# Performance work log

Hardware: AMD Instinct MI355X
Metric: run time of the kernel (lower is better)

The kernel has to match this reference:

```python
import jax, jax.numpy as jnp
import numpy as np

T, B, IN, OUT = 32, 16, 64, 64
L, W, S = 4096, 64, 3          # mem_length, mem_width, shifting_size
READ_SIZE = W + 3 + S           # k, beta, g, gamma, s
WRITE_SIZE = W + 3 + S + 2 * W  # addressing params + erase + add


def setup_inputs() -> dict:
    key = jax.random.key(0)
    k1, k2 = jax.random.split(key)
    inputs = jax.random.normal(k1, (T, B, IN), dtype=jnp.float32)
    Wc = jax.random.normal(k2, (IN + OUT + W, OUT + READ_SIZE + WRITE_SIZE), dtype=jnp.float32) * 0.05
    bc = jnp.zeros((OUT + READ_SIZE + WRITE_SIZE,), dtype=jnp.float32)
    return {"inputs": inputs, "Wc": Wc, "bc": bc}


def _get_w(params, w_prev, memory):
    # params: [B, W+3+S]; w_prev: [B, L]; memory: [B, L, W]
    k = params[:, :W]
    beta = jax.nn.softplus(params[:, W])[:, None]
    g = jax.nn.sigmoid(params[:, W + 1])[:, None]
    gamma = jax.nn.softplus(params[:, W + 2])[:, None] + 1.0
    s = jax.nn.softmax(params[:, -S:], axis=-1)
    eps = 1e-14
    norm_k = jnp.sqrt(jnp.sum(k * k, axis=-1, keepdims=True) + eps)    # [B,1]
    norm_mem = jnp.sqrt(jnp.sum(memory * memory, axis=-1) + eps)       # [B,L]
    K = jnp.einsum('blw,bw->bl', memory, k) / (norm_mem * norm_k)      # cosine sim
    w_c = jax.nn.softmax(K * beta, axis=-1)
    w_g = w_c * g + (1.0 - g) * w_prev
    # circular shift: w_tilde[i] = sum_j s[j] * w_g[(i + j - left) mod L]
    left = S // 2
    shifted = jnp.stack([jnp.roll(w_g, left - j, axis=1) for j in range(S)], axis=-1)  # [B,L,S]
    w_tilde = jnp.einsum('bls,bs->bl', shifted, s)
    w = jnp.power(w_tilde, gamma)   # sharpen, gamma >= 1
    return w / jnp.sum(w, axis=1, keepdims=True)


def reference(inputs, Wc, bc):
    Bsz = inputs.shape[1]
    r0 = jnp.zeros((Bsz, W), jnp.float32)
    o0 = jnp.zeros((Bsz, OUT), jnp.float32)
    w0 = jnp.zeros((Bsz, L), jnp.float32).at[:, 0].set(1.0)  # one-hot init weights
    m0 = jnp.zeros((Bsz, L, W), jnp.float32)

    def step(carry, x_t):
        r, out, rw, ww, mem = carry
        co = jnp.concatenate([x_t, out, r], axis=1) @ Wc + bc  # linear controller
        out = co[:, :OUT]
        rp = co[:, OUT:OUT + READ_SIZE]
        wp = co[:, -WRITE_SIZE:]
        # read head (uses pre-write memory)
        rw = _get_w(rp, rw, mem)
        r = jnp.einsum('blw,bl->bw', mem, rw)
        # write head: address with same memory, then erase/add
        ww = _get_w(wp[:, :-2 * W], ww, mem)
        e = jax.nn.sigmoid(wp[:, -2 * W:-W])
        a = wp[:, -W:]
        mem = mem * (1.0 - ww[:, :, None] * e[:, None, :]) + ww[:, :, None] * a[:, None, :]
        return (r, out, rw, ww, mem), out

    _, outs = jax.lax.scan(step, (r0, o0, w0, w0, m0), inputs)
    return outs  # [T, B, OUT]
```

## Files before the change

kernel.cpp:

```cpp
#include <hip/hip_runtime.h>

#define T_STEPS 32
#define BATCH   16
#define NBPB    8
#define NBLK    (BATCH * NBPB)
#define NTHR    1024
#define LSL     512
#define MSTR    65
#define NIN     192
#define CO      332

#define OFF_CTR   0
#define OFF_SSUM  512
#define OFF_RSUM  (OFF_SSUM + BATCH * T_STEPS * 4)
#define OFF_HE    (OFF_RSUM + BATCH * T_STEPS * 64)
#define OFF_HP    (OFF_HE + BATCH * T_STEPS * NBPB * 4)
#define COMM_FLOATS (OFF_HP + BATCH * (T_STEPS + 1) * NBPB * 4)

__device__ __forceinline__ float waveSum(float v) {
#pragma unroll
  for (int off = 32; off > 0; off >>= 1) v += __shfl_xor(v, off, 64);
  return v;
}
__device__ __forceinline__ float sigmoidf(float x) { return 1.f / (1.f + __expf(-x)); }
__device__ __forceinline__ float softplusf(float x) { return x > 15.f ? x : log1pf(__expf(x)); }
__device__ __forceinline__ float aload(const float* p) {
  return __hip_atomic_load(p, __ATOMIC_RELAXED, __HIP_MEMORY_SCOPE_AGENT);
}
__device__ __forceinline__ void astore(float* p, float v) {
  __hip_atomic_store(p, v, __ATOMIC_RELAXED, __HIP_MEMORY_SCOPE_AGENT);
}

__device__ __forceinline__ void gbar(unsigned* c, unsigned expected) {
  __syncthreads();
  if (threadIdx.x == 0) {
    atomicAdd(c, 1u);
    while (__hip_atomic_load(c, __ATOMIC_RELAXED, __HIP_MEMORY_SCOPE_AGENT) < expected)
      __builtin_amdgcn_s_sleep(1);
  }
  __syncthreads();
}

__global__ void __launch_bounds__(NTHR, 1) ntm_kernel(
    const float* __restrict__ inp, const float* __restrict__ Wc,
    const float* __restrict__ bcv, float* __restrict__ dout,
    float* __restrict__ comm)
{
  const int b   = blockIdx.x & 15;
  const int g   = blockIdx.x >> 4;
  const int tid = threadIdx.x;
  const int wv  = tid >> 6;
  const int lane = tid & 63;

  __shared__ float mem[LSL * MSTR];
  __shared__ float wpR[LSL], wpW[LSL];
  __shared__ float wbR[LSL], wbW[LSL];
  __shared__ float erR[LSL], erW[LSL];
  __shared__ float xin[NIN], kr[64], kw[64], psc[12], elds[64], alds[64];
  __shared__ float outb[2][64], scrA[16], scrB[16], red[8], rpart[64];
  __shared__ float edge[8], coef[12];

  unsigned* ctr = (unsigned*)comm + b * 32;

  for (int i = tid; i < LSL * MSTR; i += NTHR) mem[i] = 0.f;
  if (tid < LSL) { wpR[tid] = 0.f; wpW[tid] = 0.f; }
  if (g == 0 && tid == 0) { wpR[0] = 1.f; wpW[0] = 1.f; }
  if (tid < 64) { outb[0][tid] = 0.f; outb[1][tid] = 0.f; }
  {
    float* hp0 = comm + OFF_HP + ((size_t)(b * (T_STEPS + 1) + 0) * NBPB + g) * 4;
    if (tid == 0)       { float v = (g == 0) ? 1.f : 0.f; astore(hp0 + 0, v); astore(hp0 + 2, v); }
    if (tid == LSL - 1) { astore(hp0 + 1, 0.f); astore(hp0 + 3, 0.f); }
  }
  unsigned expct = NBPB;
  gbar(ctr, expct);

  for (int t = 0; t < T_STEPS; ++t) {
    float* sS  = comm + OFF_SSUM + (size_t)(b * T_STEPS + t) * 4;
    float* rS  = comm + OFF_RSUM + (size_t)(b * T_STEPS + t) * 64;
    float* hE  = comm + OFF_HE + ((size_t)(b * T_STEPS + t) * NBPB + g) * 4;
    float* hPn = comm + OFF_HP + ((size_t)(b * (T_STEPS + 1) + t + 1) * NBPB + g) * 4;

    if (tid < 64)       xin[tid] = inp[((size_t)t * BATCH + b) * 64 + tid];
    else if (tid < 128) xin[tid] = outb[(t + 1) & 1][tid - 64];
    else if (tid < 192) {
      if (t == 0) xin[tid] = 0.f;
      else {
        const float* sP = comm + OFF_SSUM + (size_t)(b * T_STEPS + t - 1) * 4;
        const float* rP = comm + OFF_RSUM + (size_t)(b * T_STEPS + t - 1) * 64;
        xin[tid] = aload(rP + (tid - 128)) / aload(sP + 2);
      }
    }
    __syncthreads();

    if (tid < 2 * CO) {
      const int col = tid >> 1, h = tid & 1;
      float acc = h ? 0.f : bcv[col];
      const float* wcp = Wc + col + (size_t)(96 * h) * CO;
#pragma unroll 8
      for (int i = 0; i < 96; ++i) acc = fmaf(xin[96 * h + i], wcp[(size_t)i * CO], acc);
      acc += __shfl_xor(acc, 1, 64);
      if (h == 0) {
        if (col < 64) {
          outb[t & 1][col] = acc;
          if (g == 0) dout[((size_t)t * BATCH + b) * 64 + col] = acc;
        }
        else if (col < 128) kr[col - 64] = acc;
        else if (col < 134) psc[col - 128] = acc;
        else if (col < 198) kw[col - 134] = acc;
        else if (col < 204) psc[6 + (col - 198)] = acc;
        else if (col < 268) elds[col - 204] = sigmoidf(acc);
        else                alds[col - 268] = acc;
      }
    }
    __syncthreads();
    if (wv == 0)      { float v = kr[lane]; float s = waveSum(v * v); if (!lane) red[4] = 1.f / sqrtf(s + 1e-14f); }
    else if (wv == 1) { float v = kw[lane]; float s = waveSum(v * v); if (!lane) red[5] = 1.f / sqrtf(s + 1e-14f); }
    else if (wv == 2 && !lane) { red[6] = softplusf(psc[0]); red[7] = softplusf(psc[6]); }
    __syncthreads();

    {
      const float invnkR = red[4], invnkW = red[5];
      const float betaR = red[6], betaW = red[7];
      const int l = tid >> 1, h = tid & 1;
      const int base = l * MSTR + 32 * h;
      const float* krh = kr + 32 * h;
      const float* kwh = kw + 32 * h;
      float ss = 0.f, dr = 0.f, dw = 0.f;
#pragma unroll 8
      for (int i = 0; i < 32; ++i) {
        float v = mem[base + i];
        ss = fmaf(v, v, ss); dr = fmaf(v, krh[i], dr); dw = fmaf(v, kwh[i], dw);
      }
      ss += __shfl_xor(ss, 1, 64);
      dr += __shfl_xor(dr, 1, 64);
      dw += __shfl_xor(dw, 1, 64);
      float rinv = rsqrtf(ss + 1e-14f);
      float eRv = __expf(betaR * (dr * rinv * invnkR - 1.f));
      float eWv = __expf(betaW * (dw * rinv * invnkW - 1.f));
      if (h == 0) {
        erR[l] = eRv; erW[l] = eWv;
        if (l == 0)       { astore(hE + 0, eRv); astore(hE + 2, eWv); }
        if (l == LSL - 1) { astore(hE + 1, eRv); astore(hE + 3, eWv); }
      }
      float sRl = h ? 0.f : eRv, sWl = h ? 0.f : eWv;
      sRl = waveSum(sRl); sWl = waveSum(sWl);
      if (!lane) { scrA[wv] = sRl; scrB[wv] = sWl; }
      __syncthreads();
      if (tid == 0) {
        float a = 0.f, bb = 0.f;
        for (int j = 0; j < 16; ++j) { a += scrA[j]; bb += scrB[j]; }
        atomicAdd(sS + 0, a); atomicAdd(sS + 1, bb);
      }
    }
    expct += NBPB; gbar(ctr, expct);

    {
      const int gm = (g + NBPB - 1) & 7, gp = (g + 1) & 7;
      if (tid == 0) {
        float invSR = 1.f / aload(sS + 0), invSW = 1.f / aload(sS + 1);
        float gR = sigmoidf(psc[1]); coef[0] = gR * invSR; coef[1] = 1.f - gR;
        coef[2] = softplusf(psc[2]) + 1.f;
        float x0 = psc[3], x1 = psc[4], x2 = psc[5];
        float mx = fmaxf(x0, fmaxf(x1, x2));
        float e0 = __expf(x0 - mx), e1 = __expf(x1 - mx), e2 = __expf(x2 - mx);
        float es = 1.f / (e0 + e1 + e2);
        coef[3] = e0 * es; coef[4] = e1 * es; coef[5] = e2 * es;
        float gW = sigmoidf(psc[7]); coef[6] = gW * invSW; coef[7] = 1.f - gW;
        coef[8] = softplusf(psc[8]) + 1.f;
        float y0 = psc[9], y1 = psc[10], y2 = psc[11];
        float my = fmaxf(y0, fmaxf(y1, y2));
        float f0 = __expf(y0 - my), f1 = __expf(y1 - my), f2 = __expf(y2 - my);
        float fs = 1.f / (f0 + f1 + f2);
        coef[9] = f0 * fs; coef[10] = f1 * fs; coef[11] = f2 * fs;
      }
      if (tid == 1) {
        const float* hEm = comm + OFF_HE + ((size_t)(b * T_STEPS + t) * NBPB + gm) * 4;
        const float* hPm = comm + OFF_HP + ((size_t)(b * (T_STEPS + 1) + t) * NBPB + gm) * 4;
        edge[0] = aload(hEm + 1); edge[1] = aload(hEm + 3);
        edge[2] = aload(hPm + 1); edge[3] = aload(hPm + 3);
      }
      if (tid == 2) {
        const float* hEp = comm + OFF_HE + ((size_t)(b * T_STEPS + t) * NBPB + gp) * 4;
        const float* hPp = comm + OFF_HP + ((size_t)(b * (T_STEPS + 1) + t) * NBPB + gp) * 4;
        edge[4] = aload(hEp + 0); edge[5] = aload(hEp + 2);
        edge[6] = aload(hPp + 0); edge[7] = aload(hPp + 2);
      }
      __syncthreads();

      float pRl = 0.f, pWl = 0.f;
      if (tid < LSL) {
        const float aR = coef[0], bR = coef[1], gaR = coef[2];
        const float sr0 = coef[3], sr1 = coef[4], sr2 = coef[5];
        const float aW = coef[6], bW = coef[7], gaW = coef[8];
        const float sw0 = coef[9], sw1 = coef[10], sw2 = coef[11];

        float erm = tid ? erR[tid - 1] : edge[0];
        float ewm = tid ? erW[tid - 1] : edge[1];
        float prm = tid ? wpR[tid - 1] : edge[2];
        float pwm = tid ? wpW[tid - 1] : edge[3];
        float erp = (tid < LSL - 1) ? erR[tid + 1] : edge[4];
        float ewp = (tid < LSL - 1) ? erW[tid + 1] : edge[5];
        float prp = (tid < LSL - 1) ? wpR[tid + 1] : edge[6];
        float pwp = (tid < LSL - 1) ? wpW[tid + 1] : edge[7];

        float wgm = aR * erm + bR * prm;
        float wg0 = aR * erR[tid] + bR * wpR[tid];
        float wgp = aR * erp + bR * prp;
        float wR = __powf(sr0 * wgm + sr1 * wg0 + sr2 * wgp, gaR);
        float vgm = aW * ewm + bW * pwm;
        float vg0 = aW * erW[tid] + bW * wpW[tid];
        float vgp = aW * ewp + bW * pwp;
        float wW = __powf(sw0 * vgm + sw1 * vg0 + sw2 * vgp, gaW);
        wbR[tid] = wR; wbW[tid] = wW;
        pRl = wR; pWl = wW;
      }
      pRl = waveSum(pRl); pWl = waveSum(pWl);
      if (!lane && wv < 8) { scrA[wv] = pRl; scrB[wv] = pWl; }
      __syncthreads();
      if (tid == 0) {
        float a = 0.f, bb = 0.f;
        for (int j = 0; j < 8; ++j) { a += scrA[j]; bb += scrB[j]; }
        atomicAdd(sS + 2, a); atomicAdd(sS + 3, bb);
      }
      float wbv[8];
#pragma unroll
      for (int k = 0; k < 8; ++k) wbv[k] = wbR[lane + 64 * k];
#pragma unroll
      for (int r2 = 0; r2 < 4; ++r2) {
        const int w = wv * 4 + r2;
        float racc = 0.f;
#pragma unroll
        for (int k = 0; k < 8; ++k)
          racc = fmaf(mem[(lane + 64 * k) * MSTR + w], wbv[k], racc);
        racc = waveSum(racc);
        if (!lane) rpart[w] = racc;
      }
      __syncthreads();
      if (tid < 64) atomicAdd(rS + tid, rpart[tid]);
    }
    expct += NBPB; gbar(ctr, expct);

    {
      if (tid == 0) { red[2] = 1.f / aload(sS + 2); red[3] = 1.f / aload(sS + 3); }
      __syncthreads();
      if (tid < LSL) {
        float nR = wbR[tid] * red[2];
        float nW = wbW[tid] * red[3];
        wpR[tid] = nR; wpW[tid] = nW;
        if (tid == 0)       { astore(hPn + 0, nR); astore(hPn + 2, nW); }
        if (tid == LSL - 1) { astore(hPn + 1, nR); astore(hPn + 3, nW); }
      }
      __syncthreads();
      float wwv[8];
#pragma unroll
      for (int k = 0; k < 8; ++k) wwv[k] = wpW[lane + 64 * k];
#pragma unroll
      for (int r2 = 0; r2 < 4; ++r2) {
        const int w = wv * 4 + r2;
        const float e_w = elds[w], a_w = alds[w];
#pragma unroll
        for (int k = 0; k < 8; ++k) {
          const int idx = (lane + 64 * k) * MSTR + w;
          float v = mem[idx];
          float nv = fmaf(v, -(wwv[k] * e_w), v);
          mem[idx] = fmaf(wwv[k], a_w, nv);
        }
      }
    }
  }
}

extern "C" void kernel_launch(void* const* d_in, const int* in_sizes, int n_in,
                              void* d_out, int out_size, void* d_ws, size_t ws_size,
                              hipStream_t stream) {
  const float* inp = (const float*)d_in[0];
  const float* Wc  = (const float*)d_in[1];
  const float* bcv = (const float*)d_in[2];
  float* dout = (float*)d_out;
  float* comm = (float*)d_ws;

  hipMemsetAsync(comm, 0, (size_t)COMM_FLOATS * sizeof(float), stream);

  void* args[] = { (void*)&inp, (void*)&Wc, (void*)&bcv, (void*)&dout, (void*)&comm };
  hipLaunchCooperativeKernel((void*)ntm_kernel, dim3(NBLK), dim3(NTHR),
                             args, 0, stream);
}
```

Baseline: 712.4 us.

## Restructure NTM step loop with overlapped controller, swizzled float4 memory, split barriers

Rewrites the per-step loop in several ways. Barrier arrival and waiting are split so the next step's controller matmul over input and output runs while waiting for peer blocks. The read-vector part of the Wc weights is cached in registers. Memory rows are padded to 68 floats with an XOR swizzle so float4 LDS accesses avoid bank conflicts. Coefficient computation is spread across threads instead of serialized on single threads, and the read reduction now goes straight to global atomics. Register pressure increases and atomic traffic per block goes up, and the swizzle and reorder add correctness risk.

```diff
diff --git a/kernel.cpp b/kernel.cpp
--- a/kernel.cpp
+++ b/kernel.cpp
@@ -6,7 +6,7 @@
 #define NBLK    (BATCH * NBPB)
 #define NTHR    1024
 #define LSL     512
-#define MSTR    65
+#define MSTR    68
 #define NIN     192
 #define CO      332
 
@@ -30,15 +30,9 @@
 __device__ __forceinline__ void astore(float* p, float v) {
   __hip_atomic_store(p, v, __ATOMIC_RELAXED, __HIP_MEMORY_SCOPE_AGENT);
 }
-
-__device__ __forceinline__ void gbar(unsigned* c, unsigned expected) {
-  __syncthreads();
-  if (threadIdx.x == 0) {
-    atomicAdd(c, 1u);
-    while (__hip_atomic_load(c, __ATOMIC_RELAXED, __HIP_MEMORY_SCOPE_AGENT) < expected)
-      __builtin_amdgcn_s_sleep(1);
-  }
-  __syncthreads();
+__device__ __forceinline__ void spin_until(const unsigned* c, unsigned expected) {
+  while (__hip_atomic_load(c, __ATOMIC_RELAXED, __HIP_MEMORY_SCOPE_AGENT) < expected)
+    __builtin_amdgcn_s_sleep(1);
 }
 
 __global__ void __launch_bounds__(NTHR, 1) ntm_kernel(
@@ -46,90 +40,127 @@
     const float* __restrict__ bcv, float* __restrict__ dout,
     float* __restrict__ comm)
 {
-  const int b   = blockIdx.x & 15;
-  const int g   = blockIdx.x >> 4;
-  const int tid = threadIdx.x;
-  const int wv  = tid >> 6;
+  const int b    = blockIdx.x & 15;
+  const int g    = blockIdx.x >> 4;
+  const int tid  = threadIdx.x;
+  const int wv   = tid >> 6;
   const int lane = tid & 63;
 
-  __shared__ float mem[LSL * MSTR];
+  __shared__ __align__(16) float mem[LSL * MSTR];
   __shared__ float wpR[LSL], wpW[LSL];
   __shared__ float wbR[LSL], wbW[LSL];
   __shared__ float erR[LSL], erW[LSL];
-  __shared__ float xin[NIN], kr[64], kw[64], psc[12], elds[64], alds[64];
-  __shared__ float outb[2][64], scrA[16], scrB[16], red[8], rpart[64];
-  __shared__ float edge[8], coef[12];
+  __shared__ __align__(16) float xin[NIN];
+  __shared__ __align__(16) float kr[64], kw[64], elds[64], alds[64];
+  __shared__ float psc[12], outb[64], scrA[16], scrB[16];
 
   unsigned* ctr = (unsigned*)comm + b * 32;
 
-  for (int i = tid; i < LSL * MSTR; i += NTHR) mem[i] = 0.f;
+  const int col  = tid >> 1;
+  const int hh   = tid & 1;
+  const bool gthr = (col < CO);
+
+  float wreg[32];
+  if (gthr) {
+#pragma unroll
+    for (int i = 0; i < 32; ++i)
+      wreg[i] = Wc[(size_t)(128 + 32 * hh + i) * CO + col];
+  }
+
+  {
+    float4 z4; z4.x = z4.y = z4.z = z4.w = 0.f;
+    float4* m4 = (float4*)mem;
+    for (int i = tid; i < (LSL * MSTR) / 4; i += NTHR) m4[i] = z4;
+  }
   if (tid < LSL) { wpR[tid] = 0.f; wpW[tid] = 0.f; }
   if (g == 0 && tid == 0) { wpR[0] = 1.f; wpW[0] = 1.f; }
-  if (tid < 64) { outb[0][tid] = 0.f; outb[1][tid] = 0.f; }
+  if (tid < 64)            xin[tid] = inp[(size_t)b * 64 + tid];
+  else if (tid < NIN)      xin[tid] = 0.f;
   {
-    float* hp0 = comm + OFF_HP + ((size_t)(b * (T_STEPS + 1) + 0) * NBPB + g) * 4;
-    if (tid == 0)       { float v = (g == 0) ? 1.f : 0.f; astore(hp0 + 0, v); astore(hp0 + 2, v); }
-    if (tid == LSL - 1) { astore(hp0 + 1, 0.f); astore(hp0 + 3, 0.f); }
+    float* hp0 = comm + OFF_HP + ((size_t)(b * (T_STEPS + 1)) * NBPB + g) * 4;
+    if (tid == 0) { float v = (g == 0) ? 1.f : 0.f; astore(hp0 + 0, v); astore(hp0 + 2, v); }
+    if (tid == 1) { astore(hp0 + 1, 0.f); astore(hp0 + 3, 0.f); }
   }
   unsigned expct = NBPB;
-  gbar(ctr, expct);
+  __syncthreads();
+  if (tid == 0)
+    __hip_atomic_fetch_add(ctr, 1u, __ATOMIC_RELEASE, __HIP_MEMORY_SCOPE_AGENT);
+  spin_until(ctr, expct);
+
+  float acc = 0.f;
+  if (gthr) {
+    acc = hh ? 0.f : bcv[col];
+    const float* wcx = Wc + col + (size_t)(64 * hh) * CO;
+#pragma unroll 4
+    for (int q = 0; q < 16; ++q) {
+      const float4 xv = *(const float4*)(xin + 64 * hh + 4 * q);
+      acc = fmaf(xv.x, wcx[(size_t)(4 * q + 0) * CO], acc);
+      acc = fmaf(xv.y, wcx[(size_t)(4 * q + 1) * CO], acc);
+      acc = fmaf(xv.z, wcx[(size_t)(4 * q + 2) * CO], acc);
+      acc = fmaf(xv.w, wcx[(size_t)(4 * q + 3) * CO], acc);
+    }
+#pragma unroll
+    for (int q = 0; q < 8; ++q) {
+      const float4 xv = *(const float4*)(xin + 128 + 32 * hh + 4 * q);
+      acc = fmaf(xv.x, wreg[4 * q + 0], acc);
+      acc = fmaf(xv.y, wreg[4 * q + 1], acc);
+      acc = fmaf(xv.z, wreg[4 * q + 2], acc);
+      acc = fmaf(xv.w, wreg[4 * q + 3], acc);
+    }
+  }
+
+  const int gm = (g + NBPB - 1) & 7, gp = (g + 1) & 7;
 
   for (int t = 0; t < T_STEPS; ++t) {
-    float* sS  = comm + OFF_SSUM + (size_t)(b * T_STEPS + t) * 4;
-    float* rS  = comm + OFF_RSUM + (size_t)(b * T_STEPS + t) * 64;
-    float* hE  = comm + OFF_HE + ((size_t)(b * T_STEPS + t) * NBPB + g) * 4;
-    float* hPn = comm + OFF_HP + ((size_t)(b * (T_STEPS + 1) + t + 1) * NBPB + g) * 4;
-
-    if (tid < 64)       xin[tid] = inp[((size_t)t * BATCH + b) * 64 + tid];
-    else if (tid < 128) xin[tid] = outb[(t + 1) & 1][tid - 64];
-    else if (tid < 192) {
-      if (t == 0) xin[tid] = 0.f;
-      else {
-        const float* sP = comm + OFF_SSUM + (size_t)(b * T_STEPS + t - 1) * 4;
-        const float* rP = comm + OFF_RSUM + (size_t)(b * T_STEPS + t - 1) * 64;
-        xin[tid] = aload(rP + (tid - 128)) / aload(sP + 2);
-      }
-    }
-    __syncthreads();
-
-    if (tid < 2 * CO) {
-      const int col = tid >> 1, h = tid & 1;
-      float acc = h ? 0.f : bcv[col];
-      const float* wcp = Wc + col + (size_t)(96 * h) * CO;
-#pragma unroll 8
-      for (int i = 0; i < 96; ++i) acc = fmaf(xin[96 * h + i], wcp[(size_t)i * CO], acc);
-      acc += __shfl_xor(acc, 1, 64);
-      if (h == 0) {
+    float* sS        = comm + OFF_SSUM + (size_t)(b * T_STEPS + t) * 4;
+    float* rS        = comm + OFF_RSUM + (size_t)(b * T_STEPS + t) * 64;
+    float* hE        = comm + OFF_HE + ((size_t)(b * T_STEPS + t) * NBPB + g) * 4;
+    float* hPn       = comm + OFF_HP + ((size_t)(b * (T_STEPS + 1) + t + 1) * NBPB + g) * 4;
+    const float* hEm = comm + OFF_HE + ((size_t)(b * T_STEPS + t) * NBPB + gm) * 4;
+    const float* hPm = comm + OFF_HP + ((size_t)(b * (T_STEPS + 1) + t) * NBPB + gm) * 4;
+    const float* hEp = comm + OFF_HE + ((size_t)(b * T_STEPS + t) * NBPB + gp) * 4;
+    const float* hPp = comm + OFF_HP + ((size_t)(b * (T_STEPS + 1) + t) * NBPB + gp) * 4;
+
+    if (gthr) {
+      float v = acc + __shfl_xor(acc, 1, 64);
+      if (hh == 0) {
         if (col < 64) {
-          outb[t & 1][col] = acc;
-          if (g == 0) dout[((size_t)t * BATCH + b) * 64 + col] = acc;
+          outb[col] = v;
+          if (g == 0) dout[((size_t)t * BATCH + b) * 64 + col] = v;
         }
-        else if (col < 128) kr[col - 64] = acc;
-        else if (col < 134) psc[col - 128] = acc;
-        else if (col < 198) kw[col - 134] = acc;
-        else if (col < 204) psc[6 + (col - 198)] = acc;
-        else if (col < 268) elds[col - 204] = sigmoidf(acc);
-        else                alds[col - 268] = acc;
-      }
-    }
-    __syncthreads();
-    if (wv == 0)      { float v = kr[lane]; float s = waveSum(v * v); if (!lane) red[4] = 1.f / sqrtf(s + 1e-14f); }
-    else if (wv == 1) { float v = kw[lane]; float s = waveSum(v * v); if (!lane) red[5] = 1.f / sqrtf(s + 1e-14f); }
-    else if (wv == 2 && !lane) { red[6] = softplusf(psc[0]); red[7] = softplusf(psc[6]); }
-    __syncthreads();
-
-    {
-      const float invnkR = red[4], invnkW = red[5];
-      const float betaR = red[6], betaW = red[7];
+        else if (col < 128) kr[col - 64] = v;
+        else if (col < 134) psc[col - 128] = v;
+        else if (col < 198) kw[col - 134] = v;
+        else if (col < 204) psc[6 + (col - 198)] = v;
+        else if (col < 268) elds[col - 204] = sigmoidf(v);
+        else                alds[col - 268] = v;
+      }
+    }
+    __syncthreads();
+
+    {
+      float vr = kr[lane]; float nr = waveSum(vr * vr);
+      float vw = kw[lane]; float nw = waveSum(vw * vw);
+      const float invnkR = rsqrtf(nr + 1e-14f);
+      const float invnkW = rsqrtf(nw + 1e-14f);
+      const float betaR = softplusf(psc[0]), betaW = softplusf(psc[6]);
+
       const int l = tid >> 1, h = tid & 1;
-      const int base = l * MSTR + 32 * h;
-      const float* krh = kr + 32 * h;
-      const float* kwh = kw + 32 * h;
+      const int x4 = ((l >> 3) & 3) << 2;
+      const float* mrow = mem + l * MSTR;
       float ss = 0.f, dr = 0.f, dw = 0.f;
-#pragma unroll 8
-      for (int i = 0; i < 32; ++i) {
-        float v = mem[base + i];
-        ss = fmaf(v, v, ss); dr = fmaf(v, krh[i], dr); dw = fmaf(v, kwh[i], dw);
+#pragma unroll
+      for (int q = 0; q < 8; ++q) {
+        const int gg = 8 * h + q;
+        const float4 v  = *(const float4*)(mrow + ((4 * gg) ^ x4));
+        const float4 ka = *(const float4*)(kr + 4 * gg);
+        const float4 kb = *(const float4*)(kw + 4 * gg);
+        ss = fmaf(v.x, v.x, ss); ss = fmaf(v.y, v.y, ss);
+        ss = fmaf(v.z, v.z, ss); ss = fmaf(v.w, v.w, ss);
+        dr = fmaf(v.x, ka.x, dr); dr = fmaf(v.y, ka.y, dr);
+        dr = fmaf(v.z, ka.z, dr); dr = fmaf(v.w, ka.w, dr);
+        dw = fmaf(v.x, kb.x, dw); dw = fmaf(v.y, kb.y, dw);
+        dw = fmaf(v.z, kb.z, dw); dw = fmaf(v.w, kb.w, dw);
       }
       ss += __shfl_xor(ss, 1, 64);
       dr += __shfl_xor(dr, 1, 64);
@@ -142,131 +173,143 @@
         if (l == 0)       { astore(hE + 0, eRv); astore(hE + 2, eWv); }
         if (l == LSL - 1) { astore(hE + 1, eRv); astore(hE + 3, eWv); }
       }
-      float sRl = h ? 0.f : eRv, sWl = h ? 0.f : eWv;
-      sRl = waveSum(sRl); sWl = waveSum(sWl);
+      float sRl = waveSum(h ? 0.f : eRv);
+      float sWl = waveSum(h ? 0.f : eWv);
       if (!lane) { scrA[wv] = sRl; scrB[wv] = sWl; }
-      __syncthreads();
-      if (tid == 0) {
-        float a = 0.f, bb = 0.f;
-        for (int j = 0; j < 16; ++j) { a += scrA[j]; bb += scrB[j]; }
-        atomicAdd(sS + 0, a); atomicAdd(sS + 1, bb);
-      }
-    }
-    expct += NBPB; gbar(ctr, expct);
-
-    {
-      const int gm = (g + NBPB - 1) & 7, gp = (g + 1) & 7;
-      if (tid == 0) {
-        float invSR = 1.f / aload(sS + 0), invSW = 1.f / aload(sS + 1);
-        float gR = sigmoidf(psc[1]); coef[0] = gR * invSR; coef[1] = 1.f - gR;
-        coef[2] = softplusf(psc[2]) + 1.f;
-        float x0 = psc[3], x1 = psc[4], x2 = psc[5];
-        float mx = fmaxf(x0, fmaxf(x1, x2));
-        float e0 = __expf(x0 - mx), e1 = __expf(x1 - mx), e2 = __expf(x2 - mx);
-        float es = 1.f / (e0 + e1 + e2);
-        coef[3] = e0 * es; coef[4] = e1 * es; coef[5] = e2 * es;
-        float gW = sigmoidf(psc[7]); coef[6] = gW * invSW; coef[7] = 1.f - gW;
-        coef[8] = softplusf(psc[8]) + 1.f;
-        float y0 = psc[9], y1 = psc[10], y2 = psc[11];
-        float my = fmaxf(y0, fmaxf(y1, y2));
-        float f0 = __expf(y0 - my), f1 = __expf(y1 - my), f2 = __expf(y2 - my);
-        float fs = 1.f / (f0 + f1 + f2);
-        coef[9] = f0 * fs; coef[10] = f1 * fs; coef[11] = f2 * fs;
-      }
-      if (tid == 1) {
-        const float* hEm = comm + OFF_HE + ((size_t)(b * T_STEPS + t) * NBPB + gm) * 4;
-        const float* hPm = comm + OFF_HP + ((size_t)(b * (T_STEPS + 1) + t) * NBPB + gm) * 4;
-        edge[0] = aload(hEm + 1); edge[1] = aload(hEm + 3);
-        edge[2] = aload(hPm + 1); edge[3] = aload(hPm + 3);
-      }
-      if (tid == 2) {
-        const float* hEp = comm + OFF_HE + ((size_t)(b * T_STEPS + t) * NBPB + gp) * 4;
-        const float* hPp = comm + OFF_HP + ((size_t)(b * (T_STEPS + 1) + t) * NBPB + gp) * 4;
-        edge[4] = aload(hEp + 0); edge[5] = aload(hEp + 2);
-        edge[6] = aload(hPp + 0); edge[7] = aload(hPp + 2);
-      }
-      __syncthreads();
-
-      float pRl = 0.f, pWl = 0.f;
-      if (tid < LSL) {
-        const float aR = coef[0], bR = coef[1], gaR = coef[2];
-        const float sr0 = coef[3], sr1 = coef[4], sr2 = coef[5];
-        const float aW = coef[6], bW = coef[7], gaW = coef[8];
-        const float sw0 = coef[9], sw1 = coef[10], sw2 = coef[11];
-
-        float erm = tid ? erR[tid - 1] : edge[0];
-        float ewm = tid ? erW[tid - 1] : edge[1];
-        float prm = tid ? wpR[tid - 1] : edge[2];
-        float pwm = tid ? wpW[tid - 1] : edge[3];
-        float erp = (tid < LSL - 1) ? erR[tid + 1] : edge[4];
-        float ewp = (tid < LSL - 1) ? erW[tid + 1] : edge[5];
-        float prp = (tid < LSL - 1) ? wpR[tid + 1] : edge[6];
-        float pwp = (tid < LSL - 1) ? wpW[tid + 1] : edge[7];
-
-        float wgm = aR * erm + bR * prm;
-        float wg0 = aR * erR[tid] + bR * wpR[tid];
-        float wgp = aR * erp + bR * prp;
-        float wR = __powf(sr0 * wgm + sr1 * wg0 + sr2 * wgp, gaR);
-        float vgm = aW * ewm + bW * pwm;
-        float vg0 = aW * erW[tid] + bW * wpW[tid];
-        float vgp = aW * ewp + bW * pwp;
-        float wW = __powf(sw0 * vgm + sw1 * vg0 + sw2 * vgp, gaW);
-        wbR[tid] = wR; wbW[tid] = wW;
-        pRl = wR; pWl = wW;
-      }
-      pRl = waveSum(pRl); pWl = waveSum(pWl);
-      if (!lane && wv < 8) { scrA[wv] = pRl; scrB[wv] = pWl; }
-      __syncthreads();
-      if (tid == 0) {
-        float a = 0.f, bb = 0.f;
-        for (int j = 0; j < 8; ++j) { a += scrA[j]; bb += scrB[j]; }
-        atomicAdd(sS + 2, a); atomicAdd(sS + 3, bb);
-      }
-      float wbv[8];
-#pragma unroll
-      for (int k = 0; k < 8; ++k) wbv[k] = wbR[lane + 64 * k];
-#pragma unroll
-      for (int r2 = 0; r2 < 4; ++r2) {
-        const int w = wv * 4 + r2;
-        float racc = 0.f;
-#pragma unroll
-        for (int k = 0; k < 8; ++k)
-          racc = fmaf(mem[(lane + 64 * k) * MSTR + w], wbv[k], racc);
-        racc = waveSum(racc);
-        if (!lane) rpart[w] = racc;
-      }
-      __syncthreads();
-      if (tid < 64) atomicAdd(rS + tid, rpart[tid]);
-    }
-    expct += NBPB; gbar(ctr, expct);
-
-    {
-      if (tid == 0) { red[2] = 1.f / aload(sS + 2); red[3] = 1.f / aload(sS + 3); }
-      __syncthreads();
-      if (tid < LSL) {
-        float nR = wbR[tid] * red[2];
-        float nW = wbW[tid] * red[3];
-        wpR[tid] = nR; wpW[tid] = nW;
-        if (tid == 0)       { astore(hPn + 0, nR); astore(hPn + 2, nW); }
-        if (tid == LSL - 1) { astore(hPn + 1, nR); astore(hPn + 3, nW); }
-      }
-      __syncthreads();
-      float wwv[8];
-#pragma unroll
-      for (int k = 0; k < 8; ++k) wwv[k] = wpW[lane + 64 * k];
-#pragma unroll
-      for (int r2 = 0; r2 < 4; ++r2) {
-        const int w = wv * 4 + r2;
-        const float e_w = elds[w], a_w = alds[w];
-#pragma unroll
-        for (int k = 0; k < 8; ++k) {
-          const int idx = (lane + 64 * k) * MSTR + w;
-          float v = mem[idx];
-          float nv = fmaf(v, -(wwv[k] * e_w), v);
-          mem[idx] = fmaf(wwv[k], a_w, nv);
-        }
-      }
-    }
+    }
+    __syncthreads();
+    if (tid == 0) {
+      float a = 0.f, bb = 0.f;
+#pragma unroll
+      for (int j = 0; j < 16; ++j) { a += scrA[j]; bb += scrB[j]; }
+      atomicAdd(sS + 0, a); atomicAdd(sS + 1, bb);
+      __hip_atomic_fetch_add(ctr, 1u, __ATOMIC_RELEASE, __HIP_MEMORY_SCOPE_AGENT);
+    }
+    expct += NBPB;
+    spin_until(ctr, expct);
+
+    {
+      const int l = tid >> 1, h = tid & 1;
+      const float S = aload(sS + h);
+      const float gg_ = sigmoidf(psc[6 * h + 1]);
+      const float aH = gg_ / S, bH = 1.f - gg_;
+      const float gaH = softplusf(psc[6 * h + 2]) + 1.f;
+      float x0 = psc[6 * h + 3], x1 = psc[6 * h + 4], x2 = psc[6 * h + 5];
+      float mx = fmaxf(x0, fmaxf(x1, x2));
+      float e0 = __expf(x0 - mx), e1 = __expf(x1 - mx), e2 = __expf(x2 - mx);
+      float es = 1.f / (e0 + e1 + e2);
+      const float c0 = e0 * es, c1 = e1 * es, c2 = e2 * es;
+
+      const float* er = h ? erW : erR;
+      const float* wp = h ? wpW : wpR;
+      float em, pm, ep, pp;
+      if (l == 0) { em = aload(hEm + 2 * h + 1); pm = aload(hPm + 2 * h + 1); }
+      else        { em = er[l - 1];              pm = wp[l - 1]; }
+      if (l == LSL - 1) { ep = aload(hEp + 2 * h); pp = aload(hPp + 2 * h); }
+      else              { ep = er[l + 1];          pp = wp[l + 1]; }
+
+      float wgm = aH * em + bH * pm;
+      float wg0 = aH * er[l] + bH * wp[l];
+      float wgp = aH * ep + bH * pp;
+      float wb = __powf(c0 * wgm + c1 * wg0 + c2 * wgp, gaH);
+      (h ? wbW : wbR)[l] = wb;
+      float sRl = waveSum(h ? 0.f : wb);
+      float sWl = waveSum(h ? wb : 0.f);
+      if (!lane) { scrA[wv] = sRl; scrB[wv] = sWl; }
+    }
+    {
+      const int tt = (t + 1 < T_STEPS) ? (t + 1) : (T_STEPS - 1);
+      if (tid < 64)       xin[tid] = inp[((size_t)tt * BATCH + b) * 64 + tid];
+      else if (tid < 128) xin[tid] = outb[tid - 64];
+    }
+    __syncthreads();
+
+    {
+      float4 racc; racc.x = racc.y = racc.z = racc.w = 0.f;
+#pragma unroll
+      for (int k = 0; k < 8; ++k) {
+        const int l2 = lane + 64 * k;
+        const float wbl = wbR[l2];
+        const float4 v = *(const float4*)(mem + l2 * MSTR +
+                           ((4 * wv) ^ (((l2 >> 3) & 3) << 2)));
+        racc.x = fmaf(v.x, wbl, racc.x);
+        racc.y = fmaf(v.y, wbl, racc.y);
+        racc.z = fmaf(v.z, wbl, racc.z);
+        racc.w = fmaf(v.w, wbl, racc.w);
+      }
+      racc.x = waveSum(racc.x); racc.y = waveSum(racc.y);
+      racc.z = waveSum(racc.z); racc.w = waveSum(racc.w);
+      if (!lane) {
+        atomicAdd(rS + 4 * wv + 0, racc.x);
+        atomicAdd(rS + 4 * wv + 1, racc.y);
+        atomicAdd(rS + 4 * wv + 2, racc.z);
+        atomicAdd(rS + 4 * wv + 3, racc.w);
+      }
+    }
+    __syncthreads();
+    if (tid == 0) {
+      float a = 0.f, bb = 0.f;
+#pragma unroll
+      for (int j = 0; j < 16; ++j) { a += scrA[j]; bb += scrB[j]; }
+      atomicAdd(sS + 2, a); atomicAdd(sS + 3, bb);
+      __hip_atomic_fetch_add(ctr, 1u, __ATOMIC_RELEASE, __HIP_MEMORY_SCOPE_AGENT);
+    }
+    expct += NBPB;
+    float nacc = 0.f;
+    if (gthr) {
+      nacc = hh ? 0.f : bcv[col];
+      const float* wcx = Wc + col + (size_t)(64 * hh) * CO;
+#pragma unroll 4
+      for (int q = 0; q < 16; ++q) {
+        const float4 xv = *(const float4*)(xin + 64 * hh + 4 * q);
+        nacc = fmaf(xv.x, wcx[(size_t)(4 * q + 0) * CO], nacc);
+        nacc = fmaf(xv.y, wcx[(size_t)(4 * q + 1) * CO], nacc);
+        nacc = fmaf(xv.z, wcx[(size_t)(4 * q + 2) * CO], nacc);
+        nacc = fmaf(xv.w, wcx[(size_t)(4 * q + 3) * CO], nacc);
+      }
+    }
+    spin_until(ctr, expct);
+
+    const float invPR = 1.f / aload(sS + 2);
+    const float invPW = 1.f / aload(sS + 3);
+    {
+      const int l = tid >> 1, h = tid & 1;
+      {
+        const float nv = (h ? wbW : wbR)[l] * (h ? invPW : invPR);
+        (h ? wpW : wpR)[l] = nv;
+        if (l == 0)       astore(hPn + 2 * h + 0, nv);
+        if (l == LSL - 1) astore(hPn + 2 * h + 1, nv);
+      }
+      const float wl = wbW[l] * invPW;
+      const int x4 = ((l >> 3) & 3) << 2;
+      float* mrow = mem + l * MSTR;
+#pragma unroll
+      for (int q = 0; q < 8; ++q) {
+        const int gg = 8 * h + q;
+        float* p = mrow + ((4 * gg) ^ x4);
+        float4 v = *(float4*)p;
+        const float4 e4 = *(const float4*)(elds + 4 * gg);
+        const float4 a4 = *(const float4*)(alds + 4 * gg);
+        v.x = fmaf(wl, a4.x, fmaf(-(wl * e4.x), v.x, v.x));
+        v.y = fmaf(wl, a4.y, fmaf(-(wl * e4.y), v.y, v.y));
+        v.z = fmaf(wl, a4.z, fmaf(-(wl * e4.z), v.z, v.z));
+        v.w = fmaf(wl, a4.w, fmaf(-(wl * e4.w), v.w, v.w));
+        *(float4*)p = v;
+      }
+    }
+    if (tid < 64) xin[128 + tid] = aload(rS + tid) * invPR;
+    __syncthreads();
+    if (gthr) {
+#pragma unroll
+      for (int q = 0; q < 8; ++q) {
+        const float4 xv = *(const float4*)(xin + 128 + 32 * hh + 4 * q);
+        nacc = fmaf(xv.x, wreg[4 * q + 0], nacc);
+        nacc = fmaf(xv.y, wreg[4 * q + 1], nacc);
+        nacc = fmaf(xv.z, wreg[4 * q + 2], nacc);
+        nacc = fmaf(xv.w, wreg[4 * q + 3], nacc);
+      }
+    }
+    acc = nacc;
   }
 }
 
```

After: 890.1 us. 1.25x slower.
